# Kernel optimization log

Hardware: AMD Instinct MI355X
Metric: run time of the kernel (lower is better)

Reference implementation:

```python
import jax, jax.numpy as jnp
import numpy as np

N = 20000   # nodes
E = 320000  # edges
F = 64      # input node features
H = 256     # hidden_layer_size
C = 10      # nbr_classes
G = 64      # graphs in the batch


def _lin(key, fan_in, fan_out):
    k1, k2 = jax.random.split(key)
    bound = 1.0 / np.sqrt(fan_in)
    W = jax.random.uniform(k1, (fan_in, fan_out), jnp.float32, -bound, bound)
    b = jax.random.uniform(k2, (fan_out,), jnp.float32, -bound, bound)
    return W, b


def setup_inputs() -> dict:
    key = jax.random.key(0)
    ks = jax.random.split(key, 10)
    x = jax.random.normal(ks[0], (N, F), jnp.float32)
    edge_index = jax.random.randint(ks[1], (2, E), 0, N)
    batch = jnp.sort(jax.random.randint(ks[2], (N,), 0, G))
    W1, b1 = _lin(ks[3], F, H)
    W2, b2 = _lin(ks[4], H, H)
    W3, b3 = _lin(ks[5], H, H)
    W4, b4 = _lin(ks[6], H, H)
    W5, b5 = _lin(ks[7], H, H)
    Wout, bout = _lin(ks[8], H, C)
    return {"x": x, "edge_index": edge_index, "batch": batch,
            "W1": W1, "b1": b1, "W2": W2, "b2": b2, "W3": W3, "b3": b3,
            "W4": W4, "b4": b4, "W5": W5, "b5": b5, "Wout": Wout, "bout": bout}


def reference(x, edge_index, batch, W1, b1, W2, b2, W3, b3, W4, b4, W5, b5, Wout, bout):
    # GCNConv (Kipf & Welling): add self-loops, D^{-1/2}(A+I)D^{-1/2} (X W) + b.
    # Dropout(p=0.5) is identity in eval mode (reference is deterministic).
    loop = jnp.arange(N)
    row = jnp.concatenate([edge_index[0], loop])  # source nodes, [E+N]
    col = jnp.concatenate([edge_index[1], loop])  # target nodes, [E+N]
    deg = jax.ops.segment_sum(jnp.ones(E + N, x.dtype), col, num_segments=N)
    dinv = jax.lax.rsqrt(deg)  # deg >= 1 thanks to self-loops
    norm = (dinv[row] * dinv[col])[:, None]  # [E+N, 1]

    def gcn_conv(h, W, b):
        m = (h @ W)[row] * norm                      # gather + normalize, [E+N, H]
        return jax.ops.segment_sum(m, col, num_segments=N) + b

    h = x
    for W, b in ((W1, b1), (W2, b2), (W3, b3), (W4, b4), (W5, b5)):
        h = jax.nn.relu(gcn_conv(h, W, b))

    # global_mean_pool over graph ids
    counts = jax.ops.segment_sum(jnp.ones(N, h.dtype), batch, num_segments=G)
    pooled = jax.ops.segment_sum(h, batch, num_segments=G) / jnp.maximum(counts, 1.0)[:, None]
    return pooled @ Wout + bout  # [G, C]
```

## Files before the change

kernel.cpp:

```cpp
#include <hip/hip_runtime.h>

#define NN 20000
#define NE 320000
#define FIN 64
#define HD 256
#define NC 10
#define NG 64

typedef unsigned short u16;
typedef unsigned int u32;
typedef __attribute__((ext_vector_type(8))) short short8;
typedef __attribute__((ext_vector_type(4))) float f32x4;

__device__ __forceinline__ float bf2f(u16 u) {
    union { u32 i; float f; } v; v.i = ((u32)u) << 16; return v.f;
}
__device__ __forceinline__ u16 f2bf(float f) {
    union { float f; u32 i; } v; v.f = f;
    u32 r = v.i + 0x7fffu + ((v.i >> 16) & 1u);
    return (u16)(r >> 16);
}

__global__ void k_prep(const float* __restrict__ x, u16* __restrict__ hx,
                       int* __restrict__ degi, int* __restrict__ gstart) {
    int i = blockIdx.x * 256 + threadIdx.x;
    if (i < NN) degi[i] = 0;
    if (i < NG) gstart[i] = NN;
    if (i < NN * FIN / 4) {
        float4 v = *(const float4*)&x[(size_t)i * 4];
        u32 lo = (u32)f2bf(v.x) | ((u32)f2bf(v.y) << 16);
        u32 hi = (u32)f2bf(v.z) | ((u32)f2bf(v.w) << 16);
        *(uint2*)&hx[(size_t)i * 4] = make_uint2(lo, hi);
    }
}

__global__ void k_deg(const int* __restrict__ col, int* __restrict__ degi,
                      const int* __restrict__ batch, int* __restrict__ gstart) {
    int i = blockIdx.x * 256 + threadIdx.x;
    if (i < NE) atomicAdd(&degi[col[i]], 1);
    if (i < NN) {
        int b = batch[i];
        int prev = (i == 0) ? -1 : batch[i - 1];
        if (b != prev) gstart[b] = i;
    }
}

__global__ __launch_bounds__(1024) void k_scan(const int* __restrict__ degi,
                                               int* __restrict__ rowptr,
                                               int* __restrict__ cursor,
                                               float* __restrict__ dinv) {
    __shared__ int wsum[16];
    __shared__ int carry;
    if (threadIdx.x == 0) carry = 0;
    __syncthreads();
    const int lane = threadIdx.x & 63;
    const int wid = threadIdx.x >> 6;
    for (int base = 0; base < NN; base += 1024) {
        int i = base + threadIdx.x;
        int v = (i < NN) ? degi[i] : 0;
        int x = v;
#pragma unroll
        for (int off = 1; off < 64; off <<= 1) {
            int y = __shfl_up(x, off);
            if (lane >= off) x += y;
        }
        if (lane == 63) wsum[wid] = x;
        __syncthreads();
        int woff = 0;
        for (int w = 0; w < wid; ++w) woff += wsum[w];
        int excl = carry + woff + x - v;
        if (i < NN) {
            rowptr[i] = excl;
            cursor[i] = excl;
            dinv[i] = rsqrtf((float)(1 + v));
        }
        __syncthreads();
        if (threadIdx.x == 0) {
            int tot = 0;
            for (int w = 0; w < 16; ++w) tot += wsum[w];
            carry += tot;
        }
        __syncthreads();
    }
    if (threadIdx.x == 0) rowptr[NN] = carry;
}

__global__ void k_fill(const int* __restrict__ row, const int* __restrict__ col,
                       int* __restrict__ cursor, int* __restrict__ ebuf) {
    int e = blockIdx.x * 256 + threadIdx.x;
    if (e < NE) {
        int c = col[e];
        int pos = atomicAdd(&cursor[c], 1);
        ebuf[pos] = row[e];
    }
}

__global__ __launch_bounds__(256) void k_trans(const float* __restrict__ W0, const float* __restrict__ W1,
                                               const float* __restrict__ W2, const float* __restrict__ W3,
                                               const float* __restrict__ W4,
                                               u16* __restrict__ T0, u16* __restrict__ T1,
                                               u16* __restrict__ T2, u16* __restrict__ T3,
                                               u16* __restrict__ T4) {
    int l = blockIdx.z;
    const float* W = (l == 0) ? W0 : (l == 1) ? W1 : (l == 2) ? W2 : (l == 3) ? W3 : W4;
    u16* T = (l == 0) ? T0 : (l == 1) ? T1 : (l == 2) ? T2 : (l == 3) ? T3 : T4;
    int K = (l == 0) ? FIN : HD;
    int k0 = blockIdx.x * 32;
    if (k0 >= K) return;
    int n0 = blockIdx.y * 32;
    __shared__ float tile[32][33];
    int tx = threadIdx.x & 31, ty = threadIdx.x >> 5;
#pragma unroll
    for (int r = 0; r < 32; r += 8)
        tile[ty + r][tx] = W[(size_t)(k0 + ty + r) * HD + n0 + tx];
    __syncthreads();
#pragma unroll
    for (int r = 0; r < 32; r += 8)
        T[(size_t)(n0 + ty + r) * K + k0 + tx] = f2bf(tile[tx][ty + r]);
}

__global__ __launch_bounds__(256) void k_mm(const u16* __restrict__ A,
                                            const u16* __restrict__ Wt,
                                            const float* __restrict__ dinv,
                                            u16* __restrict__ Y,
                                            int K) {
    __shared__ u16 Asm[64][40];
    __shared__ u16 Bsm[256][40];
    const int m0 = blockIdx.x * 64;
    const int t = threadIdx.x;
    const int wave = t >> 6;
    const int lane = t & 63;
    const int quad = lane >> 4;
    const int l16 = lane & 15;
    const int n0 = wave * 64;

    f32x4 acc[4][4];
#pragma unroll
    for (int i = 0; i < 4; ++i)
#pragma unroll
        for (int j = 0; j < 4; ++j) acc[i][j] = (f32x4){0.f, 0.f, 0.f, 0.f};

    for (int k0 = 0; k0 < K; k0 += 32) {
        {
            int row = t >> 2, seg = t & 3;
            int gm = m0 + row;
            float4 v = make_float4(0.f, 0.f, 0.f, 0.f);
            if (gm < NN) v = *(const float4*)&A[(size_t)gm * K + k0 + seg * 8];
            *(float4*)&Asm[row][seg * 8] = v;
        }
        {
#pragma unroll
            for (int j = 0; j < 4; ++j) {
                float4 v = *(const float4*)&Wt[(size_t)t * K + k0 + j * 8];
                *(float4*)&Bsm[t][j * 8] = v;
            }
        }
        __syncthreads();
        short8 a[4], b[4];
#pragma unroll
        for (int i = 0; i < 4; ++i) a[i] = *(const short8*)&Asm[i * 16 + l16][quad * 8];
#pragma unroll
        for (int j = 0; j < 4; ++j) b[j] = *(const short8*)&Bsm[n0 + j * 16 + l16][quad * 8];
#pragma unroll
        for (int i = 0; i < 4; ++i)
#pragma unroll
            for (int j = 0; j < 4; ++j)
                acc[i][j] = __builtin_amdgcn_mfma_f32_16x16x32_bf16(a[i], b[j], acc[i][j], 0, 0, 0);
        __syncthreads();
    }
#pragma unroll
    for (int i = 0; i < 4; ++i) {
#pragma unroll
        for (int r = 0; r < 4; ++r) {
            int m = m0 + i * 16 + quad * 4 + r;
            if (m >= NN) continue;
            float d = dinv[m];
#pragma unroll
            for (int j = 0; j < 4; ++j) {
                int n = n0 + j * 16 + l16;
                Y[(size_t)m * HD + n] = f2bf(acc[i][j][r] * d);
            }
        }
    }
}

__global__ __launch_bounds__(256) void k_gather(const u16* __restrict__ Y,
                                                const int* __restrict__ rowptr,
                                                const int* __restrict__ ebuf,
                                                const float* __restrict__ dinv,
                                                const float* __restrict__ b,
                                                u16* __restrict__ h) {
    int n = blockIdx.x * 4 + (threadIdx.x >> 6);
    if (n >= NN) return;
    int lane = threadIdx.x & 63;
    int half = lane >> 5;
    int seg = lane & 31;
    int s = rowptr[n], e = rowptr[n + 1];
    float acc[8];
    if (half == 0) {
        uint4 v = *(const uint4*)&Y[(size_t)n * HD + seg * 8];
        acc[0] = bf2f((u16)(v.x & 0xffff)); acc[1] = bf2f((u16)(v.x >> 16));
        acc[2] = bf2f((u16)(v.y & 0xffff)); acc[3] = bf2f((u16)(v.y >> 16));
        acc[4] = bf2f((u16)(v.z & 0xffff)); acc[5] = bf2f((u16)(v.z >> 16));
        acc[6] = bf2f((u16)(v.w & 0xffff)); acc[7] = bf2f((u16)(v.w >> 16));
    } else {
#pragma unroll
        for (int k = 0; k < 8; ++k) acc[k] = 0.f;
    }
    int j = s;
    for (; j + 4 <= e; j += 4) {
        int r0 = ebuf[j + half];
        int r1 = ebuf[j + 2 + half];
        uint4 v0 = *(const uint4*)&Y[(size_t)r0 * HD + seg * 8];
        uint4 v1 = *(const uint4*)&Y[(size_t)r1 * HD + seg * 8];
        acc[0] += bf2f((u16)(v0.x & 0xffff)); acc[1] += bf2f((u16)(v0.x >> 16));
        acc[2] += bf2f((u16)(v0.y & 0xffff)); acc[3] += bf2f((u16)(v0.y >> 16));
        acc[4] += bf2f((u16)(v0.z & 0xffff)); acc[5] += bf2f((u16)(v0.z >> 16));
        acc[6] += bf2f((u16)(v0.w & 0xffff)); acc[7] += bf2f((u16)(v0.w >> 16));
        acc[0] += bf2f((u16)(v1.x & 0xffff)); acc[1] += bf2f((u16)(v1.x >> 16));
        acc[2] += bf2f((u16)(v1.y & 0xffff)); acc[3] += bf2f((u16)(v1.y >> 16));
        acc[4] += bf2f((u16)(v1.z & 0xffff)); acc[5] += bf2f((u16)(v1.z >> 16));
        acc[6] += bf2f((u16)(v1.w & 0xffff)); acc[7] += bf2f((u16)(v1.w >> 16));
    }
    for (; j < e; j += 2) {
        int idx = j + half;
        if (idx < e) {
            int r = ebuf[idx];
            uint4 v = *(const uint4*)&Y[(size_t)r * HD + seg * 8];
            acc[0] += bf2f((u16)(v.x & 0xffff)); acc[1] += bf2f((u16)(v.x >> 16));
            acc[2] += bf2f((u16)(v.y & 0xffff)); acc[3] += bf2f((u16)(v.y >> 16));
            acc[4] += bf2f((u16)(v.z & 0xffff)); acc[5] += bf2f((u16)(v.z >> 16));
            acc[6] += bf2f((u16)(v.w & 0xffff)); acc[7] += bf2f((u16)(v.w >> 16));
        }
    }
#pragma unroll
    for (int k = 0; k < 8; ++k) acc[k] += __shfl_xor(acc[k], 32);
    if (half == 0) {
        float d = dinv[n];
        float4 b0 = *(const float4*)&b[seg * 8];
        float4 b1 = *(const float4*)&b[seg * 8 + 4];
        float r0 = fmaxf(fmaf(acc[0], d, b0.x), 0.f);
        float r1 = fmaxf(fmaf(acc[1], d, b0.y), 0.f);
        float r2 = fmaxf(fmaf(acc[2], d, b0.z), 0.f);
        float r3 = fmaxf(fmaf(acc[3], d, b0.w), 0.f);
        float r4 = fmaxf(fmaf(acc[4], d, b1.x), 0.f);
        float r5 = fmaxf(fmaf(acc[5], d, b1.y), 0.f);
        float r6 = fmaxf(fmaf(acc[6], d, b1.z), 0.f);
        float r7 = fmaxf(fmaf(acc[7], d, b1.w), 0.f);
        uint4 o;
        o.x = (u32)f2bf(r0) | ((u32)f2bf(r1) << 16);
        o.y = (u32)f2bf(r2) | ((u32)f2bf(r3) << 16);
        o.z = (u32)f2bf(r4) | ((u32)f2bf(r5) << 16);
        o.w = (u32)f2bf(r6) | ((u32)f2bf(r7) << 16);
        *(uint4*)&h[(size_t)n * HD + seg * 8] = o;
    }
}

__global__ __launch_bounds__(256) void k_poolout(const u16* __restrict__ h,
                                                 const int* __restrict__ gstart,
                                                 const float* __restrict__ Wout,
                                                 const float* __restrict__ bout,
                                                 float* __restrict__ out) {
    int g = blockIdx.x;
    int t = threadIdx.x;
    __shared__ float pooled[HD];
    __shared__ float part[NC][16];
    __shared__ int s_se[2];
    if (t == 0) {
        int st = gstart[g];
        int en = NN;
        for (int gg = g + 1; gg < NG; ++gg) en = min(en, gstart[gg]);
        s_se[0] = st; s_se[1] = en;
    }
    __syncthreads();
    int st = s_se[0], en = s_se[1];
    float a0 = 0.f, a1 = 0.f, a2 = 0.f, a3 = 0.f;
    int n = st;
    for (; n + 4 <= en; n += 4) {
        a0 += bf2f(h[(size_t)n * HD + t]);
        a1 += bf2f(h[(size_t)(n + 1) * HD + t]);
        a2 += bf2f(h[(size_t)(n + 2) * HD + t]);
        a3 += bf2f(h[(size_t)(n + 3) * HD + t]);
    }
    for (; n < en; ++n) a0 += bf2f(h[(size_t)n * HD + t]);
    float inv = 1.0f / (float)max(en - st, 1);
    pooled[t] = (a0 + a1 + a2 + a3) * inv;
    __syncthreads();
    if (t < NC * 16) {
        int c = t >> 4, l16 = t & 15;
        float s = 0.f;
        for (int f = l16; f < HD; f += 16)
            s = fmaf(pooled[f], Wout[(size_t)f * NC + c], s);
        part[c][l16] = s;
    }
    __syncthreads();
    if (t < NC) {
        float s = 0.f;
#pragma unroll
        for (int k = 0; k < 16; ++k) s += part[t][k];
        out[(size_t)g * NC + t] = s + bout[t];
    }
}

extern "C" void kernel_launch(void* const* d_in, const int* in_sizes, int n_in,
                              void* d_out, int out_size, void* d_ws, size_t ws_size,
                              hipStream_t stream) {
    const float* x     = (const float*)d_in[0];
    const int*   ei    = (const int*)d_in[1];
    const int*   batch = (const int*)d_in[2];
    const float* Wl[5] = {(const float*)d_in[3], (const float*)d_in[5], (const float*)d_in[7],
                          (const float*)d_in[9], (const float*)d_in[11]};
    const float* bl[5] = {(const float*)d_in[4], (const float*)d_in[6], (const float*)d_in[8],
                          (const float*)d_in[10], (const float*)d_in[12]};
    const float* Wout = (const float*)d_in[13];
    const float* bout = (const float*)d_in[14];
    float* out = (float*)d_out;

    const int* row = ei;
    const int* col = ei + NE;

    char* p = (char*)d_ws;
    auto take = [&](size_t bytes) { char* q = p; p += (bytes + 255) & ~(size_t)255; return q; };
    float* dinv   = (float*)take(NN * 4);
    int*   degi   = (int*)take(NN * 4);
    int*   rowptr = (int*)take((NN + 1) * 4);
    int*   cursor = (int*)take(NN * 4);
    int*   ebuf   = (int*)take(NE * 4);
    int*   gstart = (int*)take(NG * 4);
    u16*   Wt[5];
    for (int l = 0; l < 5; ++l) Wt[l] = (u16*)take((size_t)HD * HD * 2);
    u16*   hA     = (u16*)take((size_t)NN * HD * 2);
    u16*   Y      = (u16*)take((size_t)NN * HD * 2);

    k_prep<<<(NN * FIN / 4 + 255) / 256, 256, 0, stream>>>(x, hA, degi, gstart);
    k_deg<<<(NE + 255) / 256, 256, 0, stream>>>(col, degi, batch, gstart);
    k_scan<<<1, 1024, 0, stream>>>(degi, rowptr, cursor, dinv);
    k_fill<<<(NE + 255) / 256, 256, 0, stream>>>(row, col, cursor, ebuf);
    dim3 tGrid(8, 8, 5);
    k_trans<<<tGrid, 256, 0, stream>>>(Wl[0], Wl[1], Wl[2], Wl[3], Wl[4],
                                       Wt[0], Wt[1], Wt[2], Wt[3], Wt[4]);

    int K = FIN;
    for (int l = 0; l < 5; ++l) {
        k_mm<<<(NN + 63) / 64, 256, 0, stream>>>(hA, Wt[l], dinv, Y, K);
        k_gather<<<(NN + 3) / 4, 256, 0, stream>>>(Y, rowptr, ebuf, dinv, bl[l], hA);
        K = HD;
    }

    k_poolout<<<NG, 256, 0, stream>>>(hA, gstart, Wout, bout, out);
}
```

Baseline: 385.7 us.

## Aggregate before transform, gather on 64-wide input, parallelize degree scan

```diff
diff --git a/kernel.cpp b/kernel.cpp
--- a/kernel.cpp
+++ b/kernel.cpp
@@ -6,6 +6,7 @@
 #define HD 256
 #define NC 10
 #define NG 64
+#define NB ((NN + 255) / 256)
 
 typedef unsigned short u16;
 typedef unsigned int u32;
@@ -21,17 +22,10 @@
     return (u16)(r >> 16);
 }
 
-__global__ void k_prep(const float* __restrict__ x, u16* __restrict__ hx,
-                       int* __restrict__ degi, int* __restrict__ gstart) {
+__global__ void k_prep(int* __restrict__ degi, int* __restrict__ gstart) {
     int i = blockIdx.x * 256 + threadIdx.x;
     if (i < NN) degi[i] = 0;
     if (i < NG) gstart[i] = NN;
-    if (i < NN * FIN / 4) {
-        float4 v = *(const float4*)&x[(size_t)i * 4];
-        u32 lo = (u32)f2bf(v.x) | ((u32)f2bf(v.y) << 16);
-        u32 hi = (u32)f2bf(v.z) | ((u32)f2bf(v.w) << 16);
-        *(uint2*)&hx[(size_t)i * 4] = make_uint2(lo, hi);
-    }
 }
 
 __global__ void k_deg(const int* __restrict__ col, int* __restrict__ degi,
@@ -45,44 +39,62 @@
     }
 }
 
-__global__ __launch_bounds__(1024) void k_scan(const int* __restrict__ degi,
+__global__ __launch_bounds__(256) void k_scan1(const int* __restrict__ degi,
                                                int* __restrict__ rowptr,
-                                               int* __restrict__ cursor,
-                                               float* __restrict__ dinv) {
-    __shared__ int wsum[16];
-    __shared__ int carry;
-    if (threadIdx.x == 0) carry = 0;
-    __syncthreads();
-    const int lane = threadIdx.x & 63;
-    const int wid = threadIdx.x >> 6;
-    for (int base = 0; base < NN; base += 1024) {
-        int i = base + threadIdx.x;
-        int v = (i < NN) ? degi[i] : 0;
-        int x = v;
-#pragma unroll
-        for (int off = 1; off < 64; off <<= 1) {
-            int y = __shfl_up(x, off);
-            if (lane >= off) x += y;
-        }
-        if (lane == 63) wsum[wid] = x;
-        __syncthreads();
-        int woff = 0;
-        for (int w = 0; w < wid; ++w) woff += wsum[w];
-        int excl = carry + woff + x - v;
-        if (i < NN) {
-            rowptr[i] = excl;
-            cursor[i] = excl;
-            dinv[i] = rsqrtf((float)(1 + v));
-        }
-        __syncthreads();
-        if (threadIdx.x == 0) {
-            int tot = 0;
-            for (int w = 0; w < 16; ++w) tot += wsum[w];
-            carry += tot;
-        }
-        __syncthreads();
-    }
-    if (threadIdx.x == 0) rowptr[NN] = carry;
+                                               int* __restrict__ bsum) {
+    int t = threadIdx.x;
+    int i = blockIdx.x * 256 + t;
+    int v = (i < NN) ? degi[i] : 0;
+    int lane = t & 63, wid = t >> 6;
+    int x = v;
+#pragma unroll
+    for (int off = 1; off < 64; off <<= 1) {
+        int y = __shfl_up(x, off);
+        if (lane >= off) x += y;
+    }
+    __shared__ int ws[4];
+    if (lane == 63) ws[wid] = x;
+    __syncthreads();
+    int woff = 0;
+    for (int w = 0; w < wid; ++w) woff += ws[w];
+    if (i < NN) rowptr[i] = woff + x - v;
+    if (t == 255) bsum[blockIdx.x] = woff + x;
+}
+
+__global__ __launch_bounds__(128) void k_scan2(int* __restrict__ bsum, int* __restrict__ rowptr) {
+    __shared__ int s[NB + 1];
+    int t = threadIdx.x;
+    if (t < NB) s[t] = bsum[t];
+    __syncthreads();
+    if (t == 0) {
+        int run = 0;
+        for (int k = 0; k < NB; ++k) { int tmp = s[k]; s[k] = run; run += tmp; }
+        s[NB] = run;
+    }
+    __syncthreads();
+    if (t < NB) bsum[t] = s[t];
+    if (t == 0) rowptr[NN] = s[NB];
+}
+
+__global__ void k_scan3(const int* __restrict__ degi, const int* __restrict__ bsum,
+                        int* __restrict__ rowptr, int* __restrict__ cursor,
+                        float* __restrict__ dinv,
+                        const float* __restrict__ x, u16* __restrict__ u0) {
+    int i = blockIdx.x * 256 + threadIdx.x;
+    if (i < NN) {
+        int rp = rowptr[i] + bsum[i >> 8];
+        rowptr[i] = rp;
+        cursor[i] = rp;
+        dinv[i] = rsqrtf((float)(1 + degi[i]));
+    }
+    if (i < NN * FIN / 4) {
+        int node = i >> 4;
+        float d = rsqrtf((float)(1 + degi[node]));
+        float4 v = *(const float4*)&x[(size_t)i * 4];
+        u32 lo = (u32)f2bf(v.x * d) | ((u32)f2bf(v.y * d) << 16);
+        u32 hi = (u32)f2bf(v.z * d) | ((u32)f2bf(v.w * d) << 16);
+        *(uint2*)&u0[(size_t)i * 4] = make_uint2(lo, hi);
+    }
 }
 
 __global__ void k_fill(const int* __restrict__ row, const int* __restrict__ col,
@@ -119,77 +131,11 @@
         T[(size_t)(n0 + ty + r) * K + k0 + tx] = f2bf(tile[tx][ty + r]);
 }
 
-__global__ __launch_bounds__(256) void k_mm(const u16* __restrict__ A,
-                                            const u16* __restrict__ Wt,
-                                            const float* __restrict__ dinv,
-                                            u16* __restrict__ Y,
-                                            int K) {
-    __shared__ u16 Asm[64][40];
-    __shared__ u16 Bsm[256][40];
-    const int m0 = blockIdx.x * 64;
-    const int t = threadIdx.x;
-    const int wave = t >> 6;
-    const int lane = t & 63;
-    const int quad = lane >> 4;
-    const int l16 = lane & 15;
-    const int n0 = wave * 64;
-
-    f32x4 acc[4][4];
-#pragma unroll
-    for (int i = 0; i < 4; ++i)
-#pragma unroll
-        for (int j = 0; j < 4; ++j) acc[i][j] = (f32x4){0.f, 0.f, 0.f, 0.f};
-
-    for (int k0 = 0; k0 < K; k0 += 32) {
-        {
-            int row = t >> 2, seg = t & 3;
-            int gm = m0 + row;
-            float4 v = make_float4(0.f, 0.f, 0.f, 0.f);
-            if (gm < NN) v = *(const float4*)&A[(size_t)gm * K + k0 + seg * 8];
-            *(float4*)&Asm[row][seg * 8] = v;
-        }
-        {
-#pragma unroll
-            for (int j = 0; j < 4; ++j) {
-                float4 v = *(const float4*)&Wt[(size_t)t * K + k0 + j * 8];
-                *(float4*)&Bsm[t][j * 8] = v;
-            }
-        }
-        __syncthreads();
-        short8 a[4], b[4];
-#pragma unroll
-        for (int i = 0; i < 4; ++i) a[i] = *(const short8*)&Asm[i * 16 + l16][quad * 8];
-#pragma unroll
-        for (int j = 0; j < 4; ++j) b[j] = *(const short8*)&Bsm[n0 + j * 16 + l16][quad * 8];
-#pragma unroll
-        for (int i = 0; i < 4; ++i)
-#pragma unroll
-            for (int j = 0; j < 4; ++j)
-                acc[i][j] = __builtin_amdgcn_mfma_f32_16x16x32_bf16(a[i], b[j], acc[i][j], 0, 0, 0);
-        __syncthreads();
-    }
-#pragma unroll
-    for (int i = 0; i < 4; ++i) {
-#pragma unroll
-        for (int r = 0; r < 4; ++r) {
-            int m = m0 + i * 16 + quad * 4 + r;
-            if (m >= NN) continue;
-            float d = dinv[m];
-#pragma unroll
-            for (int j = 0; j < 4; ++j) {
-                int n = n0 + j * 16 + l16;
-                Y[(size_t)m * HD + n] = f2bf(acc[i][j][r] * d);
-            }
-        }
-    }
-}
-
-__global__ __launch_bounds__(256) void k_gather(const u16* __restrict__ Y,
-                                                const int* __restrict__ rowptr,
-                                                const int* __restrict__ ebuf,
-                                                const float* __restrict__ dinv,
-                                                const float* __restrict__ b,
-                                                u16* __restrict__ h) {
+__global__ __launch_bounds__(256) void k_gather256(const u16* __restrict__ U,
+                                                   const int* __restrict__ rowptr,
+                                                   const int* __restrict__ ebuf,
+                                                   const float* __restrict__ dinv,
+                                                   u16* __restrict__ Z) {
     int n = blockIdx.x * 4 + (threadIdx.x >> 6);
     if (n >= NN) return;
     int lane = threadIdx.x & 63;
@@ -198,7 +144,7 @@
     int s = rowptr[n], e = rowptr[n + 1];
     float acc[8];
     if (half == 0) {
-        uint4 v = *(const uint4*)&Y[(size_t)n * HD + seg * 8];
+        uint4 v = *(const uint4*)&U[(size_t)n * HD + seg * 8];
         acc[0] = bf2f((u16)(v.x & 0xffff)); acc[1] = bf2f((u16)(v.x >> 16));
         acc[2] = bf2f((u16)(v.y & 0xffff)); acc[3] = bf2f((u16)(v.y >> 16));
         acc[4] = bf2f((u16)(v.z & 0xffff)); acc[5] = bf2f((u16)(v.z >> 16));
@@ -207,26 +153,63 @@
 #pragma unroll
         for (int k = 0; k < 8; ++k) acc[k] = 0.f;
     }
-    int j = s;
-    for (; j + 4 <= e; j += 4) {
-        int r0 = ebuf[j + half];
-        int r1 = ebuf[j + 2 + half];
-        uint4 v0 = *(const uint4*)&Y[(size_t)r0 * HD + seg * 8];
-        uint4 v1 = *(const uint4*)&Y[(size_t)r1 * HD + seg * 8];
-        acc[0] += bf2f((u16)(v0.x & 0xffff)); acc[1] += bf2f((u16)(v0.x >> 16));
-        acc[2] += bf2f((u16)(v0.y & 0xffff)); acc[3] += bf2f((u16)(v0.y >> 16));
-        acc[4] += bf2f((u16)(v0.z & 0xffff)); acc[5] += bf2f((u16)(v0.z >> 16));
-        acc[6] += bf2f((u16)(v0.w & 0xffff)); acc[7] += bf2f((u16)(v0.w >> 16));
-        acc[0] += bf2f((u16)(v1.x & 0xffff)); acc[1] += bf2f((u16)(v1.x >> 16));
-        acc[2] += bf2f((u16)(v1.y & 0xffff)); acc[3] += bf2f((u16)(v1.y >> 16));
-        acc[4] += bf2f((u16)(v1.z & 0xffff)); acc[5] += bf2f((u16)(v1.z >> 16));
-        acc[6] += bf2f((u16)(v1.w & 0xffff)); acc[7] += bf2f((u16)(v1.w >> 16));
-    }
-    for (; j < e; j += 2) {
-        int idx = j + half;
-        if (idx < e) {
-            int r = ebuf[idx];
-            uint4 v = *(const uint4*)&Y[(size_t)r * HD + seg * 8];
+    for (int j = s; j < e; j += 16) {
+        int idx = j + half * 8 + (lane & 7);
+        int myid = (idx < e) ? ebuf[idx] : -1;
+#pragma unroll
+        for (int k = 0; k < 8; ++k) {
+            int r = __shfl(myid, (lane & 32) | k);
+            int rr = max(r, 0);
+            uint4 v = *(const uint4*)&U[(size_t)rr * HD + seg * 8];
+            if (r >= 0) {
+                acc[0] += bf2f((u16)(v.x & 0xffff)); acc[1] += bf2f((u16)(v.x >> 16));
+                acc[2] += bf2f((u16)(v.y & 0xffff)); acc[3] += bf2f((u16)(v.y >> 16));
+                acc[4] += bf2f((u16)(v.z & 0xffff)); acc[5] += bf2f((u16)(v.z >> 16));
+                acc[6] += bf2f((u16)(v.w & 0xffff)); acc[7] += bf2f((u16)(v.w >> 16));
+            }
+        }
+    }
+#pragma unroll
+    for (int k = 0; k < 8; ++k) acc[k] += __shfl_xor(acc[k], 32);
+    if (half == 0) {
+        float d = dinv[n];
+        uint4 o;
+        o.x = (u32)f2bf(acc[0] * d) | ((u32)f2bf(acc[1] * d) << 16);
+        o.y = (u32)f2bf(acc[2] * d) | ((u32)f2bf(acc[3] * d) << 16);
+        o.z = (u32)f2bf(acc[4] * d) | ((u32)f2bf(acc[5] * d) << 16);
+        o.w = (u32)f2bf(acc[6] * d) | ((u32)f2bf(acc[7] * d) << 16);
+        *(uint4*)&Z[(size_t)n * HD + seg * 8] = o;
+    }
+}
+
+__global__ __launch_bounds__(256) void k_gather64(const u16* __restrict__ U,
+                                                  const int* __restrict__ rowptr,
+                                                  const int* __restrict__ ebuf,
+                                                  const float* __restrict__ dinv,
+                                                  u16* __restrict__ Z) {
+    int n = blockIdx.x * 4 + (threadIdx.x >> 6);
+    if (n >= NN) return;
+    int lane = threadIdx.x & 63;
+    int grp = lane >> 3;
+    int seg = lane & 7;
+    int s = rowptr[n], e = rowptr[n + 1];
+    float acc[8];
+    if (grp == 0) {
+        uint4 v = *(const uint4*)&U[(size_t)n * FIN + seg * 8];
+        acc[0] = bf2f((u16)(v.x & 0xffff)); acc[1] = bf2f((u16)(v.x >> 16));
+        acc[2] = bf2f((u16)(v.y & 0xffff)); acc[3] = bf2f((u16)(v.y >> 16));
+        acc[4] = bf2f((u16)(v.z & 0xffff)); acc[5] = bf2f((u16)(v.z >> 16));
+        acc[6] = bf2f((u16)(v.w & 0xffff)); acc[7] = bf2f((u16)(v.w >> 16));
+    } else {
+#pragma unroll
+        for (int k = 0; k < 8; ++k) acc[k] = 0.f;
+    }
+    for (int j = s; j < e; j += 8) {
+        int idx = j + grp;
+        int r = (idx < e) ? ebuf[idx] : -1;
+        int rr = max(r, 0);
+        uint4 v = *(const uint4*)&U[(size_t)rr * FIN + seg * 8];
+        if (r >= 0) {
             acc[0] += bf2f((u16)(v.x & 0xffff)); acc[1] += bf2f((u16)(v.x >> 16));
             acc[2] += bf2f((u16)(v.y & 0xffff)); acc[3] += bf2f((u16)(v.y >> 16));
             acc[4] += bf2f((u16)(v.z & 0xffff)); acc[5] += bf2f((u16)(v.z >> 16));
@@ -234,25 +217,86 @@
         }
     }
 #pragma unroll
-    for (int k = 0; k < 8; ++k) acc[k] += __shfl_xor(acc[k], 32);
-    if (half == 0) {
+    for (int off = 8; off < 64; off <<= 1)
+#pragma unroll
+        for (int k = 0; k < 8; ++k) acc[k] += __shfl_xor(acc[k], off);
+    if (grp == 0) {
         float d = dinv[n];
-        float4 b0 = *(const float4*)&b[seg * 8];
-        float4 b1 = *(const float4*)&b[seg * 8 + 4];
-        float r0 = fmaxf(fmaf(acc[0], d, b0.x), 0.f);
-        float r1 = fmaxf(fmaf(acc[1], d, b0.y), 0.f);
-        float r2 = fmaxf(fmaf(acc[2], d, b0.z), 0.f);
-        float r3 = fmaxf(fmaf(acc[3], d, b0.w), 0.f);
-        float r4 = fmaxf(fmaf(acc[4], d, b1.x), 0.f);
-        float r5 = fmaxf(fmaf(acc[5], d, b1.y), 0.f);
-        float r6 = fmaxf(fmaf(acc[6], d, b1.z), 0.f);
-        float r7 = fmaxf(fmaf(acc[7], d, b1.w), 0.f);
         uint4 o;
-        o.x = (u32)f2bf(r0) | ((u32)f2bf(r1) << 16);
-        o.y = (u32)f2bf(r2) | ((u32)f2bf(r3) << 16);
-        o.z = (u32)f2bf(r4) | ((u32)f2bf(r5) << 16);
-        o.w = (u32)f2bf(r6) | ((u32)f2bf(r7) << 16);
-        *(uint4*)&h[(size_t)n * HD + seg * 8] = o;
+        o.x = (u32)f2bf(acc[0] * d) | ((u32)f2bf(acc[1] * d) << 16);
+        o.y = (u32)f2bf(acc[2] * d) | ((u32)f2bf(acc[3] * d) << 16);
+        o.z = (u32)f2bf(acc[4] * d) | ((u32)f2bf(acc[5] * d) << 16);
+        o.w = (u32)f2bf(acc[6] * d) | ((u32)f2bf(acc[7] * d) << 16);
+        *(uint4*)&Z[(size_t)n * FIN + seg * 8] = o;
+    }
+}
+
+__global__ __launch_bounds__(256) void k_mm(const u16* __restrict__ A,
+                                            const u16* __restrict__ Wt,
+                                            const float* __restrict__ bias,
+                                            const float* __restrict__ dinv,
+                                            u16* __restrict__ O,
+                                            int K, int scaleOut) {
+    __shared__ u16 Asm[64][40];
+    __shared__ u16 Bsm[256][40];
+    __shared__ float bs[HD];
+    const int m0 = blockIdx.x * 64;
+    const int t = threadIdx.x;
+    const int wave = t >> 6;
+    const int lane = t & 63;
+    const int quad = lane >> 4;
+    const int l16 = lane & 15;
+    const int n0 = wave * 64;
+    bs[t] = bias[t];
+
+    f32x4 acc[4][4];
+#pragma unroll
+    for (int i = 0; i < 4; ++i)
+#pragma unroll
+        for (int j = 0; j < 4; ++j) acc[i][j] = (f32x4){0.f, 0.f, 0.f, 0.f};
+
+    for (int k0 = 0; k0 < K; k0 += 32) {
+        {
+            int row = t >> 2, seg = t & 3;
+            int gm = m0 + row;
+            float4 v = make_float4(0.f, 0.f, 0.f, 0.f);
+            if (gm < NN) v = *(const float4*)&A[(size_t)gm * K + k0 + seg * 8];
+            *(float4*)&Asm[row][seg * 8] = v;
+        }
+        {
+#pragma unroll
+            for (int j = 0; j < 4; ++j) {
+                float4 v = *(const float4*)&Wt[(size_t)t * K + k0 + j * 8];
+                *(float4*)&Bsm[t][j * 8] = v;
+            }
+        }
+        __syncthreads();
+        short8 a[4], b[4];
+#pragma unroll
+        for (int i = 0; i < 4; ++i) a[i] = *(const short8*)&Asm[i * 16 + l16][quad * 8];
+#pragma unroll
+        for (int j = 0; j < 4; ++j) b[j] = *(const short8*)&Bsm[n0 + j * 16 + l16][quad * 8];
+#pragma unroll
+        for (int i = 0; i < 4; ++i)
+#pragma unroll
+            for (int j = 0; j < 4; ++j)
+                acc[i][j] = __builtin_amdgcn_mfma_f32_16x16x32_bf16(a[i], b[j], acc[i][j], 0, 0, 0);
+        __syncthreads();
+    }
+#pragma unroll
+    for (int i = 0; i < 4; ++i) {
+#pragma unroll
+        for (int r = 0; r < 4; ++r) {
+            int m = m0 + i * 16 + quad * 4 + r;
+            if (m >= NN) continue;
+            float d = scaleOut ? dinv[m] : 1.0f;
+#pragma unroll
+            for (int j = 0; j < 4; ++j) {
+                int n = n0 + j * 16 + l16;
+                float val = fmaxf(acc[i][j][r] + bs[n], 0.f) * d;
+                O[(size_t)m * HD + n] = f2bf(val);
+            }
+        }
     }
 }
 
@@ -325,27 +369,30 @@
     int*   degi   = (int*)take(NN * 4);
     int*   rowptr = (int*)take((NN + 1) * 4);
     int*   cursor = (int*)take(NN * 4);
+    int*   bsum   = (int*)take(NB * 4);
     int*   ebuf   = (int*)take(NE * 4);
     int*   gstart = (int*)take(NG * 4);
     u16*   Wt[5];
     for (int l = 0; l < 5; ++l) Wt[l] = (u16*)take((size_t)HD * HD * 2);
-    u16*   hA     = (u16*)take((size_t)NN * HD * 2);
-    u16*   Y      = (u16*)take((size_t)NN * HD * 2);
-
-    k_prep<<<(NN * FIN / 4 + 255) / 256, 256, 0, stream>>>(x, hA, degi, gstart);
+    u16*   B1     = (u16*)take((size_t)NN * HD * 2);
+    u16*   B2     = (u16*)take((size_t)NN * HD * 2);
+
+    k_prep<<<NB, 256, 0, stream>>>(degi, gstart);
     k_deg<<<(NE + 255) / 256, 256, 0, stream>>>(col, degi, batch, gstart);
-    k_scan<<<1, 1024, 0, stream>>>(degi, rowptr, cursor, dinv);
+    k_scan1<<<NB, 256, 0, stream>>>(degi, rowptr, bsum);
+    k_scan2<<<1, 128, 0, stream>>>(bsum, rowptr);
+    k_scan3<<<(NN * FIN / 4 + 255) / 256, 256, 0, stream>>>(degi, bsum, rowptr, cursor, dinv, x, B1);
     k_fill<<<(NE + 255) / 256, 256, 0, stream>>>(row, col, cursor, ebuf);
     dim3 tGrid(8, 8, 5);
     k_trans<<<tGrid, 256, 0, stream>>>(Wl[0], Wl[1], Wl[2], Wl[3], Wl[4],
                                        Wt[0], Wt[1], Wt[2], Wt[3], Wt[4]);
 
-    int K = FIN;
-    for (int l = 0; l < 5; ++l) {
-        k_mm<<<(NN + 63) / 64, 256, 0, stream>>>(hA, Wt[l], dinv, Y, K);
-        k_gather<<<(NN + 3) / 4, 256, 0, stream>>>(Y, rowptr, ebuf, dinv, bl[l], hA);
-        K = HD;
-    }
-
-    k_poolout<<<NG, 256, 0, stream>>>(hA, gstart, Wout, bout, out);
-}
+    k_gather64<<<(NN + 3) / 4, 256, 0, stream>>>(B1, rowptr, ebuf, dinv, B2);
+    k_mm<<<(NN + 63) / 64, 256, 0, stream>>>(B2, Wt[0], bl[0], dinv, B1, FIN, 1);
+    for (int l = 1; l < 5; ++l) {
+        k_gather256<<<(NN + 3) / 4, 256, 0, stream>>>(B1, rowptr, ebuf, dinv, B2);
+        k_mm<<<(NN + 63) / 64, 256, 0, stream>>>(B2, Wt[l], bl[l], dinv, B1, HD, (l < 4) ? 1 : 0);
+    }
+
+    k_poolout<<<NG, 256, 0, stream>>>(B1, gstart, Wout, bout, out);
+}
```

Result: faster. 363.2 us (-5.9%).
